# Kernel tuning notes

Measured on AMD Instinct MI355X. Metric: run time of the kernel, lower is better.

## Reference

```python
import jax, jax.numpy as jnp
import numpy as np

NB = 4
QN = -(2 ** (NB - 1))   # -8
QP = 2 ** (NB - 1) - 1  # 7
EPS = 1e-5


def _grad_scale(x, g):
    # forward: x, backward: grad * g (LSQ gradient scaling)
    return x * g + jax.lax.stop_gradient(x - x * g)


def _round_pass(x):
    # round with straight-through estimator
    return x + jax.lax.stop_gradient(jnp.round(x) - x)


def _lsq(v, alpha, qn, qp):
    # LSQ fake quantize-dequantize with learnable step size alpha
    g = 1.0 / np.sqrt(v.size * qp)
    a = _grad_scale(alpha, g)
    return _round_pass(jnp.clip(v / a, qn, qp)) * a


def _bn(x, g, b, m, v):
    # eval-mode BatchNorm2d over channel dim of NCHW
    s = (g * jax.lax.rsqrt(v + EPS))[None, :, None, None]
    return (x - m[None, :, None, None]) * s + b[None, :, None, None]


def _conv(x, w, stride, pad, groups):
    return jax.lax.conv_general_dilated(
        x, w, (stride, stride), pad,
        dimension_numbers=('NCHW', 'OIHW', 'NCHW'),
        feature_group_count=groups)


def setup_inputs() -> dict:
    key = jax.random.key(0)
    ks = jax.random.split(key, 4)
    inp, oup, hid = 96, 96, 576
    B, H, W = 32, 28, 28
    d = {}
    d['x'] = jax.random.normal(ks[0], (B, inp, H, W), jnp.float32)
    d['w1'] = jax.random.normal(ks[1], (hid, inp, 1, 1), jnp.float32) * 0.1
    d['w2'] = jax.random.normal(ks[2], (hid, 1, 3, 3), jnp.float32) * 0.1
    d['w3'] = jax.random.normal(ks[3], (oup, hid, 1, 1), jnp.float32) * 0.1
    for i, c in zip((1, 2, 3), (hid, hid, oup)):
        d[f'aw{i}'] = jnp.full((1,), 0.05, jnp.float32)  # weight step size
        d[f'ax{i}'] = jnp.full((1,), 0.5, jnp.float32)   # activation step size
        d[f'g{i}'] = jnp.ones((c,), jnp.float32)
        d[f'b{i}'] = jnp.zeros((c,), jnp.float32)
        d[f'm{i}'] = jnp.zeros((c,), jnp.float32)
        d[f'v{i}'] = jnp.ones((c,), jnp.float32)
    return d


def reference(x, w1, w2, w3, aw1, ax1, g1, b1, m1, v1,
              aw2, ax2, g2, b2, m2, v2, aw3, ax3, g3, b3, m3, v3):
    hid = w1.shape[0]
    # 1x1 expand conv (LSQ on activation and weight)
    h = _conv(_lsq(x, ax1, QN, QP), _lsq(w1, aw1, QN, QP), 1, [(0, 0), (0, 0)], 1)
    h = jnp.clip(_bn(h, g1, b1, m1, v1), 0.0, 6.0)
    # 3x3 depthwise conv, stride 1
    h = _conv(_lsq(h, ax2, QN, QP), _lsq(w2, aw2, QN, QP), 1, [(1, 1), (1, 1)], hid)
    h = jnp.clip(_bn(h, g2, b2, m2, v2), 0.0, 6.0)
    # 1x1 project conv
    h = _conv(_lsq(h, ax3, QN, QP), _lsq(w3, aw3, QN, QP), 1, [(0, 0), (0, 0)], 1)
    h = _bn(h, g3, b3, m3, v3)
    # identity residual (stride==1 and inp==oup)
    return x + h
```

## Files before the change

kernel.cpp:

```cpp
#include <hip/hip_runtime.h>

#define EPSF 1e-5f
#define MAGICF 12582912.0f
#define MLO 0x4B3FFFF8
#define MHI 0x4B400007

typedef int    int4v   __attribute__((ext_vector_type(4)));
typedef float  float4v __attribute__((ext_vector_type(4)));

#define W1P_OFF  0
#define W3P_OFF  55296
#define W2T_OFF  110592
#define S1B1_OFF 119808
#define S2B2_OFF 124416
#define S3B3_OFF 129024

#define F1S 296
#define H2S 304

__device__ __forceinline__ float lsq_q(float v, float a) {
    float t = v / a;
    t = fminf(fmaxf(t, -8.0f), 7.0f);
    return rintf(t);
}

__device__ __forceinline__ long q8pack_w(const float* w, int base, const int* idx, float a) {
    unsigned long long v = 0;
    #pragma unroll
    for (int j = 0; j < 8; ++j) {
        int q = (int)lsq_q(w[base + idx[j]], a);
        v |= (unsigned long long)(q & 255) << (8 * j);
    }
    return (long)v;
}

__global__ __launch_bounds__(128)
void prep_w(const float* __restrict__ w1, const float* __restrict__ w2,
            const float* __restrict__ w3,
            const float* aw1, const float* ax1, const float* ax2,
            const float* aw2, const float* ax3, const float* aw3,
            const float* __restrict__ g1, const float* __restrict__ b1,
            const float* __restrict__ m1, const float* __restrict__ v1,
            const float* __restrict__ g2, const float* __restrict__ b2,
            const float* __restrict__ m2, const float* __restrict__ v2,
            const float* __restrict__ g3, const float* __restrict__ b3,
            const float* __restrict__ m3, const float* __restrict__ v3,
            long* __restrict__ w1p, long* __restrict__ w3p,
            int* __restrict__ w2t,
            float* __restrict__ s1b1, float* __restrict__ s2b2,
            float* __restrict__ s3b3) {
    int id = blockIdx.x * 128 + threadIdx.x;
    const int lin[8] = {0, 1, 2, 3, 4, 5, 6, 7};
    const int prm[8] = {0, 2, 4, 6, 1, 3, 5, 7};
    if (id < 6912) {
        int l = id & 63, t = id >> 6;
        int kc = t % 3, ct = t / 3;
        int co = ct * 16 + (l & 15);
        int ci0 = kc * 32 + (l >> 4) * 8;
        w1p[id] = q8pack_w(w1, co * 96 + ci0, lin, aw1[0]);
    } else if (id < 13824) {
        int i = id - 6912;
        int l = i & 63, t = i >> 6;
        int kc = t % 18, ct = t / 18;
        int co = ct * 16 + (l & 15);
        int ci0 = kc * 32 + (l >> 4) * 8;
        w3p[i] = q8pack_w(w3, co * 576 + ci0, prm, aw3[0]);
    } else if (id < 14400) {
        int ch = id - 13824;
        int q[9];
        #pragma unroll
        for (int tp = 0; tp < 9; ++tp)
            q[tp] = (int)lsq_q(w2[ch * 9 + tp], aw2[0]) & 255;
        w2t[ch * 4 + 0] = q[0] | (q[1] << 8) | (q[2] << 16) | (q[3] << 24);
        w2t[ch * 4 + 1] = q[4] | (q[5] << 8) | (q[6] << 16) | (q[7] << 24);
        w2t[ch * 4 + 2] = q[8];
        w2t[ch * 4 + 3] = 0;
    } else if (id < 14976) {
        int c = id - 14400;
        float s = g1[c] / sqrtf(v1[c] + EPSF);
        float A = aw1[0] * ax1[0];
        float inv = 1.0f / ax2[0];
        s1b1[c] = A * s * inv;
        s1b1[576 + c] = (b1[c] - m1[c] * s) * inv;
    } else if (id < 15552) {
        int c = id - 14976;
        float s = g2[c] / sqrtf(v2[c] + EPSF);
        float A = ax2[0] * aw2[0];
        float inv = 1.0f / ax3[0];
        s2b2[c] = A * s * inv;
        s2b2[576 + c] = (b2[c] - m2[c] * s) * inv;
    } else if (id < 15648) {
        int c = id - 15552;
        float s = g3[c] / sqrtf(v3[c] + EPSF);
        float A = ax3[0] * aw3[0];
        s3b3[c] = A * s;
        s3b3[96 + c] = b3[c] - m3[c] * s;
    }
}

__global__ __launch_bounds__(448, 4)
void fused_k(const float* __restrict__ x, const long* __restrict__ w1p,
             const int* __restrict__ w2tg, const long* __restrict__ w3p,
             const float* __restrict__ ax1,
             const float* __restrict__ s1b1g, const float* __restrict__ s2b2g,
             const float* __restrict__ s3b3g, float* __restrict__ out) {
    __shared__ __align__(16) signed char h1[120 * F1S];
    __shared__ __align__(16) signed char h2[64 * H2S];
    __shared__ __align__(16) float l1[1152];
    __shared__ __align__(16) float l2[1152];
    __shared__ __align__(16) float l3[192];
    __shared__ __align__(16) int4v l2t[576];
    const int tid = threadIdx.x;
    const int w = tid >> 6, l = tid & 63;
    const int quad = l >> 4, c16 = l & 15;
    const int qh = quad >> 1, ql = quad & 1;
    const int b = blockIdx.x;
    const int r0 = blockIdx.y * 2;

    {
        const int lp = w * 16 + c16;
        const int row = lp / 28, col = lp - (lp / 28) * 28;
        const int img_row = r0 - 1 + row;
        const bool valid = (unsigned)img_row < 28u;
        const int p = min(max(img_row, 0), 27) * 28 + col;
        const float inv1 = 1.0f / ax1[0];

        float xv[3][8];
        #pragma unroll
        for (int kc = 0; kc < 3; ++kc) {
            const float* xs = x + (b * 96 + kc * 32 + quad * 8) * 784 + p;
            #pragma unroll
            for (int j = 0; j < 8; ++j) xv[kc][j] = xs[j * 784];
        }

        long* wstage = (long*)h2;
        for (int i = tid; i < 120 * F1S / 16; i += 448)
            ((int4v*)h1)[i] = (int4v){0, 0, 0, 0};
        if (tid < 288) {
            ((int4v*)l1)[tid] = ((const int4v*)s1b1g)[tid];
            ((int4v*)l2)[tid] = ((const int4v*)s2b2g)[tid];
        }
        if (tid < 48) ((int4v*)l3)[tid] = ((const int4v*)s3b3g)[tid];
        for (int i = tid; i < 576; i += 448) l2t[i] = ((const int4v*)w2tg)[i];
        for (int i = tid; i < 1152; i += 448) wstage[i] = w1p[i];
        __syncthreads();

        long bfr[3];
        #pragma unroll
        for (int kc = 0; kc < 3; ++kc) {
            unsigned long long v = 0;
            #pragma unroll
            for (int j = 0; j < 8; ++j) {
                int qi = __float_as_int(fmaf(xv[kc][j], inv1, MAGICF));
                qi = min(max(qi, MLO), MHI);
                v |= (unsigned long long)(qi & 255) << (8 * j);
            }
            bfr[kc] = (long)v;
        }
        const int pos_h = row * 30 + col + 1;

        for (int c = 0; c < 6; ++c) {
            long st0 = 0, st1 = 0, st2 = 0;
            if (c < 5) {
                const long* src = w1p + (c + 1) * 1152;
                st0 = src[tid];
                st1 = src[tid + 448];
                if (tid < 256) st2 = src[tid + 896];
            }
            const long* cur = wstage + (c & 1) * 1152;
            #pragma unroll 3
            for (int ctl = 0; ctl < 6; ++ctl) {
                const int ct = c * 6 + ctl;
                int4v acc; acc[0] = 0; acc[1] = 0; acc[2] = 0; acc[3] = 0;
                #pragma unroll
                for (int kc = 0; kc < 3; ++kc)
                    acc = __builtin_amdgcn_mfma_i32_16x16x32_i8(
                        cur[(ctl * 3 + kc) * 64 + l], bfr[kc], acc, 0, 0, 0);
                const int co0 = ct * 16 + quad * 4;
                float4v S = *(const float4v*)(l1 + co0);
                float4v B = *(const float4v*)(l1 + 576 + co0);
                int pk = 0;
                #pragma unroll
                for (int r2 = 0; r2 < 4; ++r2) {
                    float t = fmaf((float)acc[r2], S[r2], B[r2]);
                    t = __builtin_amdgcn_fmed3f(t, 0.0f, 7.0f);
                    pk |= (__float_as_int(t + MAGICF) & 15) << (4 * r2);
                }
                if (valid)
                    *(unsigned short*)(h1 + pos_h * F1S + (co0 >> 1)) = (unsigned short)pk;
            }
            if (c < 5) {
                long* dst = wstage + ((c + 1) & 1) * 1152;
                dst[tid] = st0;
                dst[tid + 448] = st1;
                if (tid < 256) dst[tid + 896] = st2;
            }
            __syncthreads();
        }
    }

    {
        const bool vald = ((c16 >> 3) == ql);
        const int mh = c16 & 7;
        const int jj = (mh >> 1) | ((mh & 1) << 2);
        const unsigned shla = 8u * (jj & 3);
        const unsigned mlo = (jj < 4) ? 0xFFFFFFFFu : 0u;
        const unsigned mhi = ~mlo;
        const unsigned vm  = vald ? 0xFFu : 0u;
        const unsigned vm4 = (vald && qh == 0) ? 0xFFu : 0u;
        const unsigned sh0 = qh * 8u;
        const unsigned sh1 = 16u + qh * 8u;

        #pragma unroll 2
        for (int t = w; t < 144; t += 7) {
            const int pt = t / 36, ct = t - (t / 36) * 36;
            const int pos = pt * 16 + c16;
            const int posc = min(pos, 55);
            const int row_in = posc / 28, col = posc - (posc / 28) * 28;
            const int choff = ct * 8 + ql * 4;
            const int4v tw = l2t[ct * 16 + c16];
            int4v acc; acc[0] = 0; acc[1] = 0; acc[2] = 0; acc[3] = 0;
            #pragma unroll
            for (int kc = 0; kc < 5; ++kc) {
                unsigned bb;
                if      (kc == 0) bb = ((unsigned)tw[0] >> sh0) & vm;
                else if (kc == 1) bb = ((unsigned)tw[0] >> sh1) & vm;
                else if (kc == 2) bb = ((unsigned)tw[1] >> sh0) & vm;
                else if (kc == 3) bb = ((unsigned)tw[1] >> sh1) & vm;
                else              bb = ((unsigned)tw[2]) & vm4;
                const unsigned pl = bb << shla;
                const long afrag = (long)(((unsigned long long)(pl & mhi) << 32)
                                          | (pl & mlo));
                const int tap = min(kc * 2 + qh, 8);
                const int dh = tap / 3 - 1, dc = tap - (tap / 3) * 3 - 1;
                const int pos_h = (row_in + 1 + dh) * 30 + (col + 1 + dc);
                const unsigned v = *(const unsigned*)(h1 + pos_h * F1S + choff);
                const unsigned lo = v & 0x0F0F0F0Fu;
                const unsigned hi = (v >> 4) & 0x0F0F0F0Fu;
                acc = __builtin_amdgcn_mfma_i32_16x16x32_i8(
                    afrag, (long)(((unsigned long long)hi << 32) | lo), acc, 0, 0, 0);
            }
            if (pos < 56) {
                const int c0 = ct * 16 + quad * 4;
                float4v S = *(const float4v*)(l2 + c0);
                float4v B = *(const float4v*)(l2 + 576 + c0);
                int pk = 0;
                #pragma unroll
                for (int r2 = 0; r2 < 4; ++r2) {
                    float tt = fmaf((float)acc[r2], S[r2], B[r2]);
                    tt = __builtin_amdgcn_fmed3f(tt, 0.0f, 7.0f);
                    pk |= (__float_as_int(tt + MAGICF) & 15) << (4 * r2);
                }
                *(unsigned short*)(h2 + pos * H2S + (c0 >> 1)) = (unsigned short)pk;
            }
        }
    }
    __syncthreads();

    #pragma unroll 2
    for (int t = w; t < 24; t += 7) {
        const int nt = t / 6, ct = t - (t / 6) * 6;
        const int nloc = nt * 16 + quad * 4;
        const int co = ct * 16 + c16;
        const int off = (b * 96 + co) * 784 + r0 * 28 + min(nloc, 52);
        const float4v xr = *(const float4v*)(x + off);
        const float S = l3[co], Bv = l3[96 + co];
        int4v acc; acc[0] = 0; acc[1] = 0; acc[2] = 0; acc[3] = 0;
        const signed char* arow = h2 + (nt * 16 + c16) * H2S + quad * 4;
        #pragma unroll 6
        for (int kc = 0; kc < 18; ++kc) {
            const unsigned va = *(const unsigned*)(arow + kc * 16);
            const unsigned lo = va & 0x0F0F0F0Fu;
            const unsigned hi = (va >> 4) & 0x0F0F0F0Fu;
            acc = __builtin_amdgcn_mfma_i32_16x16x32_i8(
                (long)(((unsigned long long)hi << 32) | lo),
                w3p[(ct * 18 + kc) * 64 + l], acc, 0, 0, 0);
        }
        if (nloc < 56) {
            float4v o;
            #pragma unroll
            for (int r2 = 0; r2 < 4; ++r2)
                o[r2] = fmaf((float)acc[r2], S, Bv) + xr[r2];
            *(float4v*)(out + off) = o;
        }
    }
}

extern "C" void kernel_launch(void* const* d_in, const int* in_sizes, int n_in,
                              void* d_out, int out_size, void* d_ws, size_t ws_size,
                              hipStream_t stream) {
    const float* x   = (const float*)d_in[0];
    const float* w1  = (const float*)d_in[1];
    const float* w2  = (const float*)d_in[2];
    const float* w3  = (const float*)d_in[3];
    const float* aw1 = (const float*)d_in[4];
    const float* ax1 = (const float*)d_in[5];
    const float* g1  = (const float*)d_in[6];
    const float* b1  = (const float*)d_in[7];
    const float* m1  = (const float*)d_in[8];
    const float* v1  = (const float*)d_in[9];
    const float* aw2 = (const float*)d_in[10];
    const float* ax2 = (const float*)d_in[11];
    const float* g2  = (const float*)d_in[12];
    const float* b2  = (const float*)d_in[13];
    const float* m2  = (const float*)d_in[14];
    const float* v2  = (const float*)d_in[15];
    const float* aw3 = (const float*)d_in[16];
    const float* ax3 = (const float*)d_in[17];
    const float* g3  = (const float*)d_in[18];
    const float* b3  = (const float*)d_in[19];
    const float* m3  = (const float*)d_in[20];
    const float* v3  = (const float*)d_in[21];

    char* ws = (char*)d_ws;
    long* w1p = (long*)(ws + W1P_OFF);
    long* w3p = (long*)(ws + W3P_OFF);
    int*  w2t = (int*)(ws + W2T_OFF);
    float* s1b1 = (float*)(ws + S1B1_OFF);
    float* s2b2 = (float*)(ws + S2B2_OFF);
    float* s3b3 = (float*)(ws + S3B3_OFF);

    float* out = (float*)d_out;

    prep_w<<<123, 128, 0, stream>>>(w1, w2, w3, aw1, ax1, ax2, aw2, ax3, aw3,
                                    g1, b1, m1, v1, g2, b2, m2, v2, g3, b3, m3, v3,
                                    w1p, w3p, w2t, s1b1, s2b2, s3b3);
    dim3 grid(32, 14);
    fused_k<<<grid, 448, 0, stream>>>(x, w1p, w2t, w3p, ax1, s1b1, s2b2, s3b3, out);
}
```

Measured before the change: 136.2 us.

## Stage project-conv weights through double-buffered LDS reusing the dead h1 region

Replaces separate shared arrays with one manually laid-out buffer so the project-conv weights can be staged in LDS, reusing the h1 region that is dead after the depthwise stage. The 1x1 project conv now loads w3 in three K-chunks via registers into two alternating LDS buffers, overlapping the global load of the next chunk with MFMA compute on the current one. Each wave also keeps four accumulators live and runs the epilogue once at the end, instead of reading w3 straight from global/L2 per tile. This adds extra barriers and register pressure under the 448x4 launch bounds.

```diff
diff --git a/kernel.cpp b/kernel.cpp
--- a/kernel.cpp
+++ b/kernel.cpp
@@ -104,12 +104,16 @@
              const float* __restrict__ ax1,
              const float* __restrict__ s1b1g, const float* __restrict__ s2b2g,
              const float* __restrict__ s3b3g, float* __restrict__ out) {
-    __shared__ __align__(16) signed char h1[120 * F1S];
-    __shared__ __align__(16) signed char h2[64 * H2S];
-    __shared__ __align__(16) float l1[1152];
-    __shared__ __align__(16) float l2[1152];
-    __shared__ __align__(16) float l3[192];
-    __shared__ __align__(16) int4v l2t[576];
+    __shared__ __align__(16) char smem[74176];
+    signed char* h1 = (signed char*)smem;
+    float*       l1 = (float*)(smem + 35520);
+    signed char* h2 = (signed char*)(smem + 40128);
+    float*       l2 = (float*)(smem + 59584);
+    float*       l3 = (float*)(smem + 64192);
+    int4v*      l2t = (int4v*)(smem + 64960);
+    long*    wstage = (long*)h2;
+    long*       w3s = (long*)smem;
+
     const int tid = threadIdx.x;
     const int w = tid >> 6, l = tid & 63;
     const int quad = l >> 4, c16 = l & 15;
@@ -133,8 +137,7 @@
             for (int j = 0; j < 8; ++j) xv[kc][j] = xs[j * 784];
         }
 
-        long* wstage = (long*)h2;
-        for (int i = tid; i < 120 * F1S / 16; i += 448)
+        for (int i = tid; i < 35520 / 16; i += 448)
             ((int4v*)h1)[i] = (int4v){0, 0, 0, 0};
         if (tid < 288) {
             ((int4v*)l1)[tid] = ((const int4v*)s1b1g)[tid];
@@ -255,33 +258,86 @@
             }
         }
     }
-    __syncthreads();
-
-    #pragma unroll 2
-    for (int t = w; t < 24; t += 7) {
-        const int nt = t / 6, ct = t - (t / 6) * 6;
-        const int nloc = nt * 16 + quad * 4;
-        const int co = ct * 16 + c16;
-        const int off = (b * 96 + co) * 784 + r0 * 28 + min(nloc, 52);
-        const float4v xr = *(const float4v*)(x + off);
-        const float S = l3[co], Bv = l3[96 + co];
-        int4v acc; acc[0] = 0; acc[1] = 0; acc[2] = 0; acc[3] = 0;
-        const signed char* arow = h2 + (nt * 16 + c16) * H2S + quad * 4;
-        #pragma unroll 6
-        for (int kc = 0; kc < 18; ++kc) {
-            const unsigned va = *(const unsigned*)(arow + kc * 16);
-            const unsigned lo = va & 0x0F0F0F0Fu;
-            const unsigned hi = (va >> 4) & 0x0F0F0F0Fu;
-            acc = __builtin_amdgcn_mfma_i32_16x16x32_i8(
-                (long)(((unsigned long long)hi << 32) | lo),
-                w3p[(ct * 18 + kc) * 64 + l], acc, 0, 0, 0);
-        }
-        if (nloc < 56) {
-            float4v o;
-            #pragma unroll
-            for (int r2 = 0; r2 < 4; ++r2)
-                o[r2] = fmaf((float)acc[r2], S, Bv) + xr[r2];
-            *(float4v*)(out + off) = o;
+
+    {
+        long stg[6];
+        auto c3_issue = [&](int ck) {
+            #pragma unroll
+            for (int k = 0; k < 6; ++k) {
+                const int e = tid + k * 448;
+                if (e < 2304) {
+                    const int ct2 = e / 384, rem = e - ct2 * 384;
+                    stg[k] = w3p[ct2 * 1152 + ck * 384 + rem];
+                }
+            }
+        };
+        auto c3_write = [&](int buf) {
+            #pragma unroll
+            for (int k = 0; k < 6; ++k) {
+                const int e = tid + k * 448;
+                if (e < 2304) w3s[buf * 2304 + e] = stg[k];
+            }
+        };
+
+        int4v accs[4];
+        #pragma unroll
+        for (int tt = 0; tt < 4; ++tt) {
+            accs[tt][0] = 0; accs[tt][1] = 0; accs[tt][2] = 0; accs[tt][3] = 0;
+        }
+        auto c3_compute = [&](int ck, int buf) {
+            #pragma unroll
+            for (int tt = 0; tt < 4; ++tt) {
+                const int t = w + tt * 7;
+                if (t < 24) {
+                    const int nt = t / 6, ct = t - (t / 6) * 6;
+                    const signed char* arow = h2 + (nt * 16 + c16) * H2S + quad * 4;
+                    #pragma unroll
+                    for (int kcl = 0; kcl < 6; ++kcl) {
+                        const int kc = ck * 6 + kcl;
+                        const unsigned va = *(const unsigned*)(arow + kc * 16);
+                        const unsigned lo = va & 0x0F0F0F0Fu;
+                        const unsigned hi = (va >> 4) & 0x0F0F0F0Fu;
+                        accs[tt] = __builtin_amdgcn_mfma_i32_16x16x32_i8(
+                            (long)(((unsigned long long)hi << 32) | lo),
+                            w3s[buf * 2304 + (ct * 6 + kcl) * 64 + l],
+                            accs[tt], 0, 0, 0);
+                    }
+                }
+            }
+        };
+
+        c3_issue(0);
+        __syncthreads();
+        c3_write(0);
+        c3_issue(1);
+        __syncthreads();
+        c3_compute(0, 0);
+        c3_write(1);
+        c3_issue(2);
+        __syncthreads();
+        c3_compute(1, 1);
+        c3_write(0);
+        __syncthreads();
+        c3_compute(2, 0);
+
+        #pragma unroll
+        for (int tt = 0; tt < 4; ++tt) {
+            const int t = w + tt * 7;
+            if (t < 24) {
+                const int nt = t / 6, ct = t - (t / 6) * 6;
+                const int nloc = nt * 16 + quad * 4;
+                const int co = ct * 16 + c16;
+                const int off = (b * 96 + co) * 784 + r0 * 28 + min(nloc, 52);
+                if (nloc < 56) {
+                    const float4v xr = *(const float4v*)(x + off);
+                    const float S = l3[co], Bv = l3[96 + co];
+                    float4v o;
+                    #pragma unroll
+                    for (int r2 = 0; r2 < 4; ++r2)
+                        o[r2] = fmaf((float)accs[tt][r2], S, Bv) + xr[r2];
+                    *(float4v*)(out + off) = o;
+                }
+            }
         }
     }
 }
```

Result: no change. 136.6 us (+0.3%).
